# Kernel optimization log

Hardware: AMD Instinct MI355X
Metric: run time of the kernel (lower is better)

Reference implementation:

```python
import jax, jax.numpy as jnp
import numpy as np

V, F, D, C = 100000, 512, 512, 128      # graph nodes, raw feat dim, internal_dim, num_classes
N1, S1, B1 = 36864, 32768, 4096         # layer-1 dstsrc / src / dst counts
S2, B2 = 3584, 512                      # layer-2 src / dst counts


def setup_inputs() -> dict:
    key = jax.random.key(0)
    ks = jax.random.split(key, 11)
    features = jax.random.normal(ks[0], (V, F), jnp.float32)
    src_nodes = jax.random.randint(ks[1], (N1,), 0, V)
    dst_idx1 = jax.random.randint(ks[2], (B1,), 0, N1)
    src_idx1 = jax.random.randint(ks[3], (S1,), 0, N1)
    # row-normalized diffusion matrix (minibatch generator produces mean-normalized adjacency)
    dif_mat1 = jax.random.uniform(ks[4], (B1, S1), jnp.float32) / S1
    dst_idx2 = jax.random.randint(ks[5], (B2,), 0, B1)
    src_idx2 = jax.random.randint(ks[6], (S2,), 0, B1)
    dif_mat2 = jax.random.uniform(ks[7], (B2, S2), jnp.float32) / S2
    # Glorot-ish weight init
    w1 = jax.random.normal(ks[8], (2 * F, D), jnp.float32) / np.float32(np.sqrt(2 * F))
    w2 = jax.random.normal(ks[9], (2 * D, D), jnp.float32) / np.float32(np.sqrt(2 * D))
    w_cls = jax.random.normal(ks[10], (D, C), jnp.float32) / np.float32(np.sqrt(D))
    return dict(features=features, src_nodes=src_nodes,
                dst_idx1=dst_idx1, src_idx1=src_idx1, dif_mat1=dif_mat1,
                dst_idx2=dst_idx2, src_idx2=src_idx2, dif_mat2=dif_mat2,
                w1=w1, w2=w2, w_cls=w_cls)


def _mean_aggregate(x, dst_idx, src_idx, dif_mat, w):
    # boolean_mask -> gather at selected indices
    agg = dif_mat @ x[src_idx]                       # [B, F_in]
    cat = jnp.concatenate([agg, x[dst_idx]], axis=1)  # [B, 2*F_in]
    return jax.nn.relu(cat @ w)                       # [B, D]


def reference(features, src_nodes, dst_idx1, src_idx1, dif_mat1,
              dst_idx2, src_idx2, dif_mat2, w1, w2, w_cls):
    x = features[src_nodes]                           # RawFeature: gather [N1, F]
    x = _mean_aggregate(x, dst_idx1, src_idx1, dif_mat1, w1)   # [B1, D]
    x = _mean_aggregate(x, dst_idx2, src_idx2, dif_mat2, w2)   # [B2, D]
    return jax.nn.softmax(x @ w_cls, axis=-1)          # classifier [B2, C]
```

## Files before the change

kernel.cpp:

```cpp
#include <hip/hip_runtime.h>

typedef unsigned short u16;
typedef unsigned int u32;
typedef __attribute__((ext_vector_type(8))) short short8;
typedef __attribute__((ext_vector_type(4))) float f32x4;
typedef __attribute__((ext_vector_type(8))) u16 ushort8v;

__device__ __forceinline__ u16 f2bf(float f) {
    union { float f; u32 u; } v; v.f = f;
    return (u16)((v.u + 0x7FFFu + ((v.u >> 16) & 1u)) >> 16);
}
__device__ __forceinline__ u32 pack2bf(float a, float b) {
    union { float f; u32 u; } x, y; x.f = a; y.f = b;
    u32 ra = x.u + 0x7FFFu + ((x.u >> 16) & 1u);
    u32 rb = y.u + 0x7FFFu + ((y.u >> 16) & 1u);
    return (ra >> 16) | (rb & 0xFFFF0000u);
}

__global__ __launch_bounds__(256) void gather_transpose_bf16(
    const float* __restrict__ src, const int* __restrict__ lvl1,
    const int* __restrict__ lvl2, u16* __restrict__ outT, int S)
{
    __shared__ u16 tile[32][514];
    const int s0 = blockIdx.x * 32;
    const int tid = threadIdx.x;
    const int r = tid >> 3;
    const int fb = (tid & 7) * 4;

    int row = lvl1[s0 + r];
    if (lvl2) row = lvl2[row];
    const float* sp = src + (size_t)row * 512;
    #pragma unroll
    for (int j = 0; j < 16; ++j) {
        float4 v = *(const float4*)(sp + fb + j * 32);
        *(u32*)&tile[r][fb + j * 32]     = pack2bf(v.x, v.y);
        *(u32*)&tile[r][fb + j * 32 + 2] = pack2bf(v.z, v.w);
    }
    __syncthreads();

    #pragma unroll
    for (int i = 0; i < 8; ++i) {
        int f = i * 64 + (tid >> 2);
        int sb = (tid & 3) * 8;
        ushort8v o;
        #pragma unroll
        for (int j = 0; j < 8; ++j) o[j] = tile[sb + j][f];
        *(ushort8v*)(outT + (size_t)f * S + s0 + sb) = o;
    }
}

__global__ __launch_bounds__(128) void gather_rows_f32(
    const float* __restrict__ src, const int* __restrict__ lvl1,
    const int* __restrict__ lvl2, float* __restrict__ out)
{
    int b = blockIdx.x;
    int row = lvl1[b];
    if (lvl2) row = lvl2[row];
    float4 v = *(const float4*)(src + (size_t)row * 512 + threadIdx.x * 4);
    *(float4*)(out + (size_t)b * 512 + threadIdx.x * 4) = v;
}

__global__ __launch_bounds__(256) void transpose_to_bf16(
    const float* __restrict__ in, u16* __restrict__ out, int R, int C)
{
    __shared__ float t[32][33];
    const int r0 = blockIdx.x * 32, c0 = blockIdx.y * 32;
    const int tr = threadIdx.x >> 3;
    const int tc = (threadIdx.x & 7) * 4;
    float4 v = *(const float4*)(in + (size_t)(r0 + tr) * C + c0 + tc);
    t[tr][tc] = v.x; t[tr][tc + 1] = v.y; t[tr][tc + 2] = v.z; t[tr][tc + 3] = v.w;
    __syncthreads();
    ushort4 o;
    o.x = f2bf(t[tc + 0][tr]); o.y = f2bf(t[tc + 1][tr]);
    o.z = f2bf(t[tc + 2][tr]); o.w = f2bf(t[tc + 3][tr]);
    *(ushort4*)(out + (size_t)(c0 + tr) * R + r0 + tc) = o;
}

__global__ __launch_bounds__(256, 3) void mfma_gemm_splitk(
    const float* __restrict__ A0, const float* __restrict__ A1, int K0,
    const u16* __restrict__ BT, float* __restrict__ part,
    int M, int N, int K)
{
    __shared__ u16 As[2][128][32];
    __shared__ u16 Bs[2][128][32];

    const int nwx = gridDim.x, nwy = gridDim.y;
    const int nwg = nwx * nwy * gridDim.z;
    const int orig = blockIdx.x + nwx * (blockIdx.y + nwy * blockIdx.z);
    const int qq = nwg >> 3, rr = nwg & 7;
    const int xcd = orig & 7;
    const int wgid = (xcd < rr ? xcd * (qq + 1) : rr * (qq + 1) + (xcd - rr) * qq)
                     + (orig >> 3);
    const int bx = wgid % nwx;
    const int tmp = wgid / nwx;
    const int by = tmp % nwy;
    const int bz = tmp / nwy;

    const int tid = threadIdx.x;
    const int n0 = bx * 128;
    const int m0 = by * 128;
    const int kchunk = K / gridDim.z;
    const int kbeg = bz * kchunk;
    const int kend = kbeg + kchunk;

    const int wave = tid >> 6, lane = tid & 63;
    const int wm = (wave >> 1) * 64;
    const int wn = (wave & 1) * 64;
    const int fm = lane & 15, q = lane >> 4;
    const int fsw = (q ^ (fm & 3)) << 3;

    const int ar = tid >> 1;
    const int ac = (tid & 1) << 4;
    const int sl0 = (tid & 1) << 1;
    const int ps0 = ((sl0 ^ (ar & 3)) << 3);
    const int ps1 = (((sl0 + 1) ^ (ar & 3)) << 3);
    const int sA1 = K - K0;

    f32x4 acc[4][4];
    #pragma unroll
    for (int i = 0; i < 4; ++i)
        #pragma unroll
        for (int j = 0; j < 4; ++j) acc[i][j] = (f32x4){0.f, 0.f, 0.f, 0.f};

    float4 v0, v1, v2, v3;
    uint4 b0, b1;

#define LOAD_TILE(k0_) do {                                                   \
    const float* ap = ((k0_) < K0)                                            \
        ? (A0 + (size_t)(m0 + ar) * K0 + (k0_) + ac)                          \
        : (A1 + (size_t)(m0 + ar) * sA1 + ((k0_) - K0) + ac);                 \
    v0 = *(const float4*)(ap);                                                \
    v1 = *(const float4*)(ap + 4);                                            \
    v2 = *(const float4*)(ap + 8);                                            \
    v3 = *(const float4*)(ap + 12);                                           \
    const u16* bp = BT + (size_t)(n0 + ar) * K + (k0_) + ac;                  \
    b0 = *(const uint4*)bp;                                                   \
    b1 = *(const uint4*)(bp + 8);                                             \
} while (0)

#define WRITE_TILE(buf_) do {                                                 \
    uint4 w0, w1;                                                             \
    w0.x = pack2bf(v0.x, v0.y); w0.y = pack2bf(v0.z, v0.w);                   \
    w0.z = pack2bf(v1.x, v1.y); w0.w = pack2bf(v1.z, v1.w);                   \
    w1.x = pack2bf(v2.x, v2.y); w1.y = pack2bf(v2.z, v2.w);                   \
    w1.z = pack2bf(v3.x, v3.y); w1.w = pack2bf(v3.z, v3.w);                   \
    *(uint4*)&As[buf_][ar][ps0] = w0;                                         \
    *(uint4*)&As[buf_][ar][ps1] = w1;                                         \
    *(uint4*)&Bs[buf_][ar][ps0] = b0;                                         \
    *(uint4*)&Bs[buf_][ar][ps1] = b1;                                         \
} while (0)

#define COMPUTE(buf_) do {                                                    \
    short8 af[4], bfr[4];                                                     \
    _Pragma("unroll")                                                         \
    for (int mi = 0; mi < 4; ++mi)                                            \
        af[mi] = *(short8*)&As[buf_][wm + mi * 16 + fm][fsw];                 \
    _Pragma("unroll")                                                         \
    for (int ni = 0; ni < 4; ++ni)                                            \
        bfr[ni] = *(short8*)&Bs[buf_][wn + ni * 16 + fm][fsw];                \
    _Pragma("unroll")                                                         \
    for (int mi = 0; mi < 4; ++mi)                                            \
        _Pragma("unroll")                                                     \
        for (int ni = 0; ni < 4; ++ni)                                        \
            acc[mi][ni] = __builtin_amdgcn_mfma_f32_16x16x32_bf16(            \
                af[mi], bfr[ni], acc[mi][ni], 0, 0, 0);                       \
} while (0)

    LOAD_TILE(kbeg);
    WRITE_TILE(0);
    __syncthreads();

    int cur = 0;
    for (int k0 = kbeg + 32; k0 < kend; k0 += 32) {
        LOAD_TILE(k0);
        COMPUTE(cur);
        WRITE_TILE(cur ^ 1);
        __syncthreads();
        cur ^= 1;
    }
    COMPUTE(cur);

#undef LOAD_TILE
#undef WRITE_TILE
#undef COMPUTE

    float* dst = part + (size_t)bz * M * N;
    #pragma unroll
    for (int mi = 0; mi < 4; ++mi)
        #pragma unroll
        for (int ni = 0; ni < 4; ++ni)
            #pragma unroll
            for (int r = 0; r < 4; ++r) {
                int row = m0 + wm + mi * 16 + q * 4 + r;
                int col = n0 + wn + ni * 16 + fm;
                dst[(size_t)row * N + col] = acc[mi][ni][r];
            }
}

template<int RELU>
__global__ __launch_bounds__(256) void reduce_partials(
    const float4* __restrict__ part, float4* __restrict__ out, int MN4, int S)
{
    int i = blockIdx.x * 256 + threadIdx.x;
    if (i >= MN4) return;
    float4 a = part[i];
    for (int s = 1; s < S; ++s) {
        float4 b = part[(size_t)s * MN4 + i];
        a.x += b.x; a.y += b.y; a.z += b.z; a.w += b.w;
    }
    if (RELU) {
        a.x = fmaxf(a.x, 0.f); a.y = fmaxf(a.y, 0.f);
        a.z = fmaxf(a.z, 0.f); a.w = fmaxf(a.w, 0.f);
    }
    out[i] = a;
}

__global__ __launch_bounds__(128) void cls_softmax(
    const float* __restrict__ h2, const float* __restrict__ wcls,
    float* __restrict__ out)
{
    __shared__ float row[512];
    __shared__ float red[128];
    const int m = blockIdx.x, c = threadIdx.x;
    *(float4*)&row[c * 4] = *(const float4*)(h2 + (size_t)m * 512 + c * 4);
    __syncthreads();
    float acc = 0.f;
    #pragma unroll 8
    for (int k = 0; k < 512; ++k) acc += row[k] * wcls[k * 128 + c];
    red[c] = acc; __syncthreads();
    for (int s = 64; s > 0; s >>= 1) {
        if (c < s) red[c] = fmaxf(red[c], red[c + s]);
        __syncthreads();
    }
    float mx = red[0]; __syncthreads();
    float e = expf(acc - mx);
    red[c] = e; __syncthreads();
    for (int s = 64; s > 0; s >>= 1) {
        if (c < s) red[c] += red[c + s];
        __syncthreads();
    }
    out[(size_t)m * 128 + c] = e / red[0];
}

extern "C" void kernel_launch(void* const* d_in, const int* in_sizes, int n_in,
                              void* d_out, int out_size, void* d_ws, size_t ws_size,
                              hipStream_t stream)
{
    (void)in_sizes; (void)n_in; (void)out_size;
    const float* features  = (const float*)d_in[0];
    const int*   src_nodes = (const int*)d_in[1];
    const int*   dst_idx1  = (const int*)d_in[2];
    const int*   src_idx1  = (const int*)d_in[3];
    const float* dif1      = (const float*)d_in[4];
    const int*   dst_idx2  = (const int*)d_in[5];
    const int*   src_idx2  = (const int*)d_in[6];
    const float* dif2      = (const float*)d_in[7];
    const float* w1        = (const float*)d_in[8];
    const float* w2        = (const float*)d_in[9];
    const float* wcls      = (const float*)d_in[10];
    float* out = (float*)d_out;

    const size_t MB = 1024ull * 1024ull;
    int splits1 = (ws_size >= 102 * MB) ? 8 : ((ws_size >= 70 * MB) ? 4 : 2);
    int splits2 = (splits1 >= 4) ? 4 : 2;

    char* ws = (char*)d_ws;
    u16*   xs1T   = (u16*)ws;
    float* agg1   = (float*)ws;
    float* xd1    = (float*)(ws + 8 * MB);
    float* h1     = (float*)(ws + 16 * MB);
    u16*   h1selT = (u16*)(ws + 24 * MB);
    float* h1dst  = (float*)(ws + 28 * MB);
    float* part   = (float*)(ws + 32 * MB);
    size_t po = 32 * MB + (size_t)splits1 * 8 * MB;
    u16*   w1T  = (u16*)(ws + po); po += MB;
    u16*   w2T  = (u16*)(ws + po); po += MB;
    float* agg2 = (float*)(ws + po); po += MB;
    float* h2   = (float*)(ws + po); po += MB;

    transpose_to_bf16<<<dim3(32, 16), 256, 0, stream>>>(w1, w1T, 1024, 512);
    transpose_to_bf16<<<dim3(32, 16), 256, 0, stream>>>(w2, w2T, 1024, 512);

    gather_transpose_bf16<<<32768 / 32, 256, 0, stream>>>(features, src_idx1, src_nodes, xs1T, 32768);

    mfma_gemm_splitk<<<dim3(4, 32, splits1), 256, 0, stream>>>(
        dif1, nullptr, 32768, xs1T, part, 4096, 512, 32768);
    reduce_partials<0><<<2048, 256, 0, stream>>>((const float4*)part, (float4*)agg1, 524288, splits1);

    gather_rows_f32<<<4096, 128, 0, stream>>>(features, dst_idx1, src_nodes, xd1);

    mfma_gemm_splitk<<<dim3(4, 32, splits2), 256, 0, stream>>>(
        agg1, xd1, 512, w1T, part, 4096, 512, 1024);
    reduce_partials<1><<<2048, 256, 0, stream>>>((const float4*)part, (float4*)h1, 524288, splits2);

    gather_transpose_bf16<<<3584 / 32, 256, 0, stream>>>(h1, src_idx2, nullptr, h1selT, 3584);
    gather_rows_f32<<<512, 128, 0, stream>>>(h1, dst_idx2, nullptr, h1dst);

    mfma_gemm_splitk<<<dim3(4, 4, 16), 256, 0, stream>>>(
        dif2, nullptr, 3584, h1selT, part, 512, 512, 3584);
    reduce_partials<0><<<256, 256, 0, stream>>>((const float4*)part, (float4*)agg2, 65536, 16);

    mfma_gemm_splitk<<<dim3(4, 4, 16), 256, 0, stream>>>(
        agg2, h1dst, 512, w2T, part, 512, 512, 1024);
    reduce_partials<1><<<256, 256, 0, stream>>>((const float4*)part, (float4*)h2, 65536, 16);

    cls_softmax<<<512, 128, 0, stream>>>(h2, wcls, out);
}
```

Baseline: 1.089 ms.

## Stream GEMM B tiles via global_load_lds with 64-deep K tiles

Restructures the split-K MFMA GEMM so the bf16 B operand is copied straight from global memory into LDS with global_load_lds. The K-step per iteration doubles to 64, with two 32-wide sub-tiles, and A is converted with the hardware v_cvt_pk_bf16_f32 instruction into a padded LDS layout instead of the XOR swizzle. Launch bounds drop to 2 blocks per CU to fit the larger LDS tiles. The two weight transposes are merged into one launch, and the layer-2 aggregation GEMM uses more K splits. The aim is to cut register staging and conversion overhead and raise bytes per iteration, at the cost of occupancy and possible LDS bank conflicts on the unswizzled B tiles.

```diff
diff --git a/kernel.cpp b/kernel.cpp
--- a/kernel.cpp
+++ b/kernel.cpp
@@ -15,6 +15,11 @@
     u32 ra = x.u + 0x7FFFu + ((x.u >> 16) & 1u);
     u32 rb = y.u + 0x7FFFu + ((y.u >> 16) & 1u);
     return (ra >> 16) | (rb & 0xFFFF0000u);
+}
+__device__ __forceinline__ u32 cvtpk(float a, float b) {
+    u32 r;
+    asm("v_cvt_pk_bf16_f32 %0, %1, %2" : "=v"(r) : "v"(a), "v"(b));
+    return r;
 }
 
 __global__ __launch_bounds__(256) void gather_transpose_bf16(
@@ -60,9 +65,13 @@
     *(float4*)(out + (size_t)b * 512 + threadIdx.x * 4) = v;
 }
 
-__global__ __launch_bounds__(256) void transpose_to_bf16(
-    const float* __restrict__ in, u16* __restrict__ out, int R, int C)
-{
+__global__ __launch_bounds__(256) void transpose2_to_bf16(
+    const float* __restrict__ inA, u16* __restrict__ outA,
+    const float* __restrict__ inB, u16* __restrict__ outB)
+{
+    const float* in = blockIdx.z ? inB : inA;
+    u16* out = blockIdx.z ? outB : outA;
+    const int R = 1024, C = 512;
     __shared__ float t[32][33];
     const int r0 = blockIdx.x * 32, c0 = blockIdx.y * 32;
     const int tr = threadIdx.x >> 3;
@@ -76,13 +85,13 @@
     *(ushort4*)(out + (size_t)(c0 + tr) * R + r0 + tc) = o;
 }
 
-__global__ __launch_bounds__(256, 3) void mfma_gemm_splitk(
+__global__ __launch_bounds__(256, 2) void mfma_gemm_splitk(
     const float* __restrict__ A0, const float* __restrict__ A1, int K0,
     const u16* __restrict__ BT, float* __restrict__ part,
     int M, int N, int K)
 {
-    __shared__ u16 As[2][128][32];
-    __shared__ u16 Bs[2][128][32];
+    __shared__ u16 As[2][2][128][40];
+    __shared__ u16 Bs[2][2][128][32];
 
     const int nwx = gridDim.x, nwy = gridDim.y;
     const int nwg = nwx * nwy * gridDim.z;
@@ -107,13 +116,9 @@
     const int wm = (wave >> 1) * 64;
     const int wn = (wave & 1) * 64;
     const int fm = lane & 15, q = lane >> 4;
-    const int fsw = (q ^ (fm & 3)) << 3;
 
     const int ar = tid >> 1;
-    const int ac = (tid & 1) << 4;
-    const int sl0 = (tid & 1) << 1;
-    const int ps0 = ((sl0 ^ (ar & 3)) << 3);
-    const int ps1 = (((sl0 + 1) ^ (ar & 3)) << 3);
+    const int ah = tid & 1;
     const int sA1 = K - K0;
 
     f32x4 acc[4][4];
@@ -122,66 +127,84 @@
         #pragma unroll
         for (int j = 0; j < 4; ++j) acc[i][j] = (f32x4){0.f, 0.f, 0.f, 0.f};
 
-    float4 v0, v1, v2, v3;
-    uint4 b0, b1;
-
-#define LOAD_TILE(k0_) do {                                                   \
-    const float* ap = ((k0_) < K0)                                            \
-        ? (A0 + (size_t)(m0 + ar) * K0 + (k0_) + ac)                          \
-        : (A1 + (size_t)(m0 + ar) * sA1 + ((k0_) - K0) + ac);                 \
-    v0 = *(const float4*)(ap);                                                \
-    v1 = *(const float4*)(ap + 4);                                            \
-    v2 = *(const float4*)(ap + 8);                                            \
-    v3 = *(const float4*)(ap + 12);                                           \
-    const u16* bp = BT + (size_t)(n0 + ar) * K + (k0_) + ac;                  \
-    b0 = *(const uint4*)bp;                                                   \
-    b1 = *(const uint4*)(bp + 8);                                             \
+    float4 av[8];
+
+#define DMA_B(k0_, buf_) do {                                                 \
+    _Pragma("unroll")                                                         \
+    for (int c = 0; c < 4; ++c) {                                             \
+        int inst = c * 4 + wave;                                              \
+        int ks = inst >> 3;                                                   \
+        int row = (inst & 7) * 16 + (lane >> 2);                              \
+        int col = (k0_) + ks * 32 + (lane & 3) * 8;                           \
+        const u16* gp = BT + (size_t)(n0 + row) * K + col;                    \
+        u16* lp = &Bs[buf_][0][0][0] + inst * 512;                            \
+        __builtin_amdgcn_global_load_lds(                                     \
+            (const __attribute__((address_space(1))) unsigned*)gp,            \
+            (__attribute__((address_space(3))) unsigned*)lp, 16, 0, 0);       \
+    }                                                                         \
 } while (0)
 
-#define WRITE_TILE(buf_) do {                                                 \
-    uint4 w0, w1;                                                             \
-    w0.x = pack2bf(v0.x, v0.y); w0.y = pack2bf(v0.z, v0.w);                   \
-    w0.z = pack2bf(v1.x, v1.y); w0.w = pack2bf(v1.z, v1.w);                   \
-    w1.x = pack2bf(v2.x, v2.y); w1.y = pack2bf(v2.z, v2.w);                   \
-    w1.z = pack2bf(v3.x, v3.y); w1.w = pack2bf(v3.z, v3.w);                   \
-    *(uint4*)&As[buf_][ar][ps0] = w0;                                         \
-    *(uint4*)&As[buf_][ar][ps1] = w1;                                         \
-    *(uint4*)&Bs[buf_][ar][ps0] = b0;                                         \
-    *(uint4*)&Bs[buf_][ar][ps1] = b1;                                         \
+#define LOAD_A(k0_) do {                                                      \
+    int kk = (k0_) + ah * 32;                                                 \
+    const float* ap = (kk < K0)                                               \
+        ? (A0 + (size_t)(m0 + ar) * K0 + kk)                                  \
+        : (A1 + (size_t)(m0 + ar) * sA1 + (kk - K0));                         \
+    _Pragma("unroll")                                                         \
+    for (int j = 0; j < 8; ++j) av[j] = *(const float4*)(ap + j * 4);         \
 } while (0)
 
+#define CVT_WRITE_A(buf_) do {                                                \
+    _Pragma("unroll")                                                         \
+    for (int s = 0; s < 4; ++s) {                                             \
+        uint4 wv;                                                             \
+        wv.x = cvtpk(av[2 * s].x,     av[2 * s].y);                           \
+        wv.y = cvtpk(av[2 * s].z,     av[2 * s].w);                           \
+        wv.z = cvtpk(av[2 * s + 1].x, av[2 * s + 1].y);                       \
+        wv.w = cvtpk(av[2 * s + 1].z, av[2 * s + 1].w);                       \
+        *(uint4*)&As[buf_][ah][ar][s * 8] = wv;                               \
+    }                                                                         \
+} while (0)
+
 #define COMPUTE(buf_) do {                                                    \
-    short8 af[4], bfr[4];                                                     \
-    _Pragma("unroll")                                                         \
-    for (int mi = 0; mi < 4; ++mi)                                            \
-        af[mi] = *(short8*)&As[buf_][wm + mi * 16 + fm][fsw];                 \
-    _Pragma("unroll")                                                         \
-    for (int ni = 0; ni < 4; ++ni)                                            \
-        bfr[ni] = *(short8*)&Bs[buf_][wn + ni * 16 + fm][fsw];                \
-    _Pragma("unroll")                                                         \
-    for (int mi = 0; mi < 4; ++mi)                                            \
+    short8 af[2][4], bfr[2][4];                                               \
+    _Pragma("unroll")                                                         \
+    for (int ks = 0; ks < 2; ++ks) {                                          \
+        _Pragma("unroll")                                                     \
+        for (int mi = 0; mi < 4; ++mi)                                        \
+            af[ks][mi] = *(short8*)&As[buf_][ks][wm + mi * 16 + fm][q * 8];   \
         _Pragma("unroll")                                                     \
         for (int ni = 0; ni < 4; ++ni)                                        \
-            acc[mi][ni] = __builtin_amdgcn_mfma_f32_16x16x32_bf16(            \
-                af[mi], bfr[ni], acc[mi][ni], 0, 0, 0);                       \
+            bfr[ks][ni] = *(short8*)&Bs[buf_][ks][wn + ni * 16 + fm][q * 8];  \
+    }                                                                         \
+    _Pragma("unroll")                                                         \
+    for (int ks = 0; ks < 2; ++ks)                                            \
+        _Pragma("unroll")                                                     \
+        for (int mi = 0; mi < 4; ++mi)                                        \
+            _Pragma("unroll")                                                 \
+            for (int ni = 0; ni < 4; ++ni)                                    \
+                acc[mi][ni] = __builtin_amdgcn_mfma_f32_16x16x32_bf16(        \
+                    af[ks][mi], bfr[ks][ni], acc[mi][ni], 0, 0, 0);           \
 } while (0)
 
-    LOAD_TILE(kbeg);
-    WRITE_TILE(0);
+    DMA_B(kbeg, 0);
+    LOAD_A(kbeg);
+    CVT_WRITE_A(0);
     __syncthreads();
 
     int cur = 0;
-    for (int k0 = kbeg + 32; k0 < kend; k0 += 32) {
-        LOAD_TILE(k0);
+    for (int k0 = kbeg + 64; k0 < kend; k0 += 64) {
+        DMA_B(k0, cur ^ 1);
+        LOAD_A(k0);
         COMPUTE(cur);
-        WRITE_TILE(cur ^ 1);
+        CVT_WRITE_A(cur ^ 1);
         __syncthreads();
         cur ^= 1;
     }
     COMPUTE(cur);
 
-#undef LOAD_TILE
-#undef WRITE_TILE
+#undef DMA_B
+#undef LOAD_A
+#undef CVT_WRITE_A
 #undef COMPUTE
 
     float* dst = part + (size_t)bz * M * N;
@@ -263,6 +286,8 @@
     const size_t MB = 1024ull * 1024ull;
     int splits1 = (ws_size >= 102 * MB) ? 8 : ((ws_size >= 70 * MB) ? 4 : 2);
     int splits2 = (splits1 >= 4) ? 4 : 2;
+    int splits3 = (splits1 >= 4) ? 28 : 14;
+    int splits4 = 16;
 
     char* ws = (char*)d_ws;
     u16*   xs1T   = (u16*)ws;
@@ -278,8 +303,7 @@
     float* agg2 = (float*)(ws + po); po += MB;
     float* h2   = (float*)(ws + po); po += MB;
 
-    transpose_to_bf16<<<dim3(32, 16), 256, 0, stream>>>(w1, w1T, 1024, 512);
-    transpose_to_bf16<<<dim3(32, 16), 256, 0, stream>>>(w2, w2T, 1024, 512);
+    transpose2_to_bf16<<<dim3(32, 16, 2), 256, 0, stream>>>(w1, w1T, w2, w2T);
 
     gather_transpose_bf16<<<32768 / 32, 256, 0, stream>>>(features, src_idx1, src_nodes, xs1T, 32768);
 
@@ -296,13 +320,13 @@
     gather_transpose_bf16<<<3584 / 32, 256, 0, stream>>>(h1, src_idx2, nullptr, h1selT, 3584);
     gather_rows_f32<<<512, 128, 0, stream>>>(h1, dst_idx2, nullptr, h1dst);
 
-    mfma_gemm_splitk<<<dim3(4, 4, 16), 256, 0, stream>>>(
+    mfma_gemm_splitk<<<dim3(4, 4, splits3), 256, 0, stream>>>(
         dif2, nullptr, 3584, h1selT, part, 512, 512, 3584);
-    reduce_partials<0><<<256, 256, 0, stream>>>((const float4*)part, (float4*)agg2, 65536, 16);
-
-    mfma_gemm_splitk<<<dim3(4, 4, 16), 256, 0, stream>>>(
+    reduce_partials<0><<<256, 256, 0, stream>>>((const float4*)part, (float4*)agg2, 65536, splits3);
+
+    mfma_gemm_splitk<<<dim3(4, 4, splits4), 256, 0, stream>>>(
         agg2, h1dst, 512, w2T, part, 512, 512, 1024);
-    reduce_partials<1><<<256, 256, 0, stream>>>((const float4*)part, (float4*)h2, 65536, 16);
+    reduce_partials<1><<<256, 256, 0, stream>>>((const float4*)part, (float4*)h2, 65536, splits4);
 
     cls_softmax<<<512, 128, 0, stream>>>(h2, wcls, out);
 }
```

New measurement: 1.206 ms. +10.7%, slower.
